# Kernel optimization log

Hardware: AMD Instinct MI355X
Metric: run time of the kernel (lower is better)

The kernel has to match this reference:

```python
import jax, jax.numpy as jnp
import numpy as np

STATE_DIM = 13
HIDDEN = 1024
NUM_SENSORS = 32
BATCH = 131072


def _sensor_locations():
    # Replicates the torch buffer construction (linspace over theta/phi on a sphere of radius 2)
    sensor_range = 2.0
    theta = np.linspace(0.0, 2.0 * np.pi, NUM_SENSORS // 2, dtype=np.float64)
    phi = np.linspace(0.0, np.pi, 2, dtype=np.float64)
    sensors = []
    for p in phi:
        for t in theta:
            sensors.append([sensor_range * np.sin(p) * np.cos(t),
                            sensor_range * np.sin(p) * np.sin(t),
                            sensor_range * np.cos(p)])
    return jnp.asarray(np.asarray(sensors[:NUM_SENSORS], dtype=np.float32))


def setup_inputs() -> dict:
    key = jax.random.key(0)
    ks = jax.random.split(key, 24)

    def lin(kw, fan_in, fan_out):
        # torch nn.Linear default init: U(-1/sqrt(fan_in), 1/sqrt(fan_in))
        bound = 1.0 / np.sqrt(fan_in)
        w = jax.random.uniform(kw, (fan_in, fan_out), jnp.float32, -bound, bound)
        return w

    def bias(kb, fan_in, fan_out):
        bound = 1.0 / np.sqrt(fan_in)
        return jax.random.uniform(kb, (fan_out,), jnp.float32, -bound, bound)

    branch_in = NUM_SENSORS * (STATE_DIM + 4)  # 544
    h2, h4, h8 = HIDDEN // 2, HIDDEN // 4, HIDDEN // 8
    inp = {
        "state": jax.random.normal(ks[0], (BATCH, STATE_DIM), jnp.float32),
        "action": jax.random.normal(ks[1], (BATCH, 4), jnp.float32),
        "sensor_locations": _sensor_locations(),
        "bw1": lin(ks[2], branch_in, HIDDEN), "bb1": bias(ks[3], branch_in, HIDDEN),
        "bw2": lin(ks[4], HIDDEN, h2), "bb2": bias(ks[5], HIDDEN, h2),
        "bw3": lin(ks[6], h2, h4), "bb3": bias(ks[7], h2, h4),
        "tw1": lin(ks[8], 3, h4), "tb1": bias(ks[9], 3, h4),
        "tw2": lin(ks[10], h4, h4), "tb2": bias(ks[11], h4, h4),
        "qw1": lin(ks[12], 3, h8), "qb1": bias(ks[13], 3, h8),
        "qw2": lin(ks[14], h8, STATE_DIM), "qb2": bias(ks[15], h8, STATE_DIM),
        "pw": lin(ks[16], h4, STATE_DIM), "pb": bias(ks[17], h4, STATE_DIM),
        "residual_weight": jnp.float32(0.1),
    }
    return inp


def reference(state, action, sensor_locations,
              bw1, bb1, bw2, bb2, bw3, bb3,
              tw1, tb1, tw2, tb2,
              qw1, qb1, qw2, qb2,
              pw, pb, residual_weight):
    B = state.shape[0]
    pos = state[:, :3]

    # Vectorized sensor encoding (replaces the 32-iteration python loop):
    # distance [B, S, 1], weight = exp(-d/0.5)
    diff = sensor_locations[None, :, :] - pos[:, None, :]          # [B, S, 3]
    dist = jnp.linalg.norm(diff, axis=-1, keepdims=True)           # [B, S, 1]
    w = jnp.exp(-dist / 0.5)                                       # [B, S, 1]
    sv = jnp.concatenate([state[:, None, :] * w,
                          action[:, None, :] * w], axis=-1)        # [B, S, sd+4]
    enc = sv.reshape(B, -1)                                        # [B, S*(sd+4)]

    # Branch net (dropout is identity in eval mode)
    h = jax.nn.relu(enc @ bw1 + bb1)
    h = jax.nn.relu(h @ bw2 + bb2)
    branch = h @ bw3 + bb3                                         # [B, hidden//4]

    # Trunk net on eval coords
    t = jnp.tanh(pos @ tw1 + tb1)
    trunk = jnp.tanh(t @ tw2 + tb2)                                # [B, hidden//4]

    interaction = branch * trunk
    output_delta = interaction @ pw + pb                           # [B, state_dim]

    b = jax.nn.relu(pos @ qw1 + qb1)
    bias_out = b @ qw2 + qb2                                       # [B, state_dim]

    next_state = state + residual_weight * (output_delta + bias_out)

    # Quaternion normalization for dims 3:7 (state_dim >= 7)
    quat = next_state[:, 3:7]
    qn = jnp.linalg.norm(quat, axis=1, keepdims=True)
    next_state = next_state.at[:, 3:7].set(quat / (qn + 1e-8))
    return next_state
```

## Files before the change

kernel.cpp:

```cpp
#include <hip/hip_runtime.h>
#include <hip/hip_bf16.h>
#include <hip/hip_fp8.h>

#define B_TOTAL 131072

typedef __attribute__((ext_vector_type(8))) short short8;
typedef __attribute__((ext_vector_type(4))) float f32x4;
typedef __attribute__((ext_vector_type(16))) unsigned char uchar16;
typedef __attribute__((ext_vector_type(4))) int int4v;
typedef __attribute__((ext_vector_type(8))) int int8v;
typedef unsigned int uint;

#define MFMA(a,b,c) __builtin_amdgcn_mfma_f32_16x16x32_bf16(a,b,c,0,0,0)
#define MFMA8(a,b,c) __builtin_amdgcn_mfma_f32_16x16x32_fp8_fp8(a,b,c,0,0,0)
#define MFMAS(a,b,c) __builtin_amdgcn_mfma_scale_f32_16x16x128_f8f6f4( \
    a, b, c, 0, 0, 0, 0x7F7F7F7F, 0, 0x7F7F7F7F)

union V8U { int8v v; int4v h[2]; };

__device__ __forceinline__ short f2bf(float f) {
  union { float f; uint u; } x; x.f = f;
  uint r = x.u + 0x7fffu + ((x.u >> 16) & 1u);
  return (short)(r >> 16);
}
__device__ __forceinline__ unsigned char f2fp8(float v) {
  union { __hip_fp8_e4m3 q; unsigned char b; } u;
  u.q = __hip_fp8_e4m3(v);
  return u.b;
}
__device__ __forceinline__ float ftanh(float x) {
  float e = __builtin_amdgcn_exp2f(x * 2.8853900817779268f);
  return 1.f - 2.f * __builtin_amdgcn_rcpf(e + 1.f);
}

__device__ __forceinline__ void gl_lds16(const void* g, void* l) {
  __builtin_amdgcn_global_load_lds((const __attribute__((address_space(1))) uint*)g,
                                   (__attribute__((address_space(3))) uint*)l, 16, 0, 0);
}
__device__ __forceinline__ int swz8(int c, int r) { return (c & ~7) | ((c ^ r) & 7); }

__global__ __launch_bounds__(256)
void prep(const float* __restrict__ bw1, const float* __restrict__ bw2,
          const float* __restrict__ bw3, const float* __restrict__ tw2,
          const float* __restrict__ pw, const float* __restrict__ qw2,
          unsigned char* __restrict__ w1f, unsigned char* __restrict__ w2f,
          unsigned char* __restrict__ w3r, short* __restrict__ w4r,
          short* __restrict__ pwT, short* __restrict__ qw2T) {
  __shared__ float tile[32][33];
  int b = blockIdx.x;
  if (b == 1344) {
    for (int t = threadIdx.x; t < 6144; t += 256) {
      if (t < 4096) { int c = t >> 8, k = t & 255;
        pwT[t] = (c < 13) ? f2bf(pw[k * 13 + c]) : (short)0; }
      else { int i = t - 4096; int c = i >> 7, j = i & 127;
        qw2T[i] = (c < 13) ? f2bf(qw2[j * 13 + c]) : (short)0; }
    }
    return;
  }
  const float* src; int K, N, mat;
  if (b < 640)       { src = bw1; K = 544;  N = 1024; mat = 0; }
  else if (b < 1152) { b -= 640;  src = bw2; K = 1024; N = 512;  mat = 1; }
  else if (b < 1280) { b -= 1152; src = bw3; K = 512;  N = 256;  mat = 2; }
  else               { b -= 1280; src = tw2; K = 256;  N = 256;  mat = 3; }
  const int ntk = (mat == 0) ? 20 : (mat == 1) ? 32 : (mat == 2) ? 16 : 8;
  const int tn = b / ntk, tk = b % ntk;
  const int k0 = tk * 32, n0 = tn * 32;
  const int tx = threadIdx.x & 31, ty = threadIdx.x >> 5;
#pragma unroll
  for (int rr = 0; rr < 32; rr += 8) {
    int k = k0 + ty + rr;
    tile[ty + rr][tx] = (k < K) ? src[(long)k * N + n0 + tx] : 0.f;
  }
  __syncthreads();
#pragma unroll
  for (int rr = 0; rr < 32; rr += 8) {
    int nl = ty + rr;
    int n = n0 + nl, k = k0 + tx;
    float v = tile[tx][nl];
    if (mat == 0) w1f[(long)n * 640 + k] = f2fp8(v);
    else if (mat == 1) w2f[(long)n * 1024 + k] = f2fp8(v);
    else {
      int ks = k >> 5, fq = (k >> 3) & 3, j = k & 7;
      int wb = n >> 5, hf = (n >> 4) & 1, fr = n & 15;
      long idx = (long)(((ks * 8 + wb) * 2 + hf) * 4 + fq) * 128 + fr * 8 + j;
      if (mat == 2) w3r[idx] = f2fp8(v);
      else          w4r[idx] = f2bf(v);
    }
  }
}

__global__ __launch_bounds__(256)
void enc_k(const float* __restrict__ state, const float* __restrict__ action,
           const float* __restrict__ sensors, unsigned char* __restrict__ enc) {
  __shared__ float sval[64][17];
  __shared__ float wexp[64][32];
  __shared__ float sens[96];
  const int tid = threadIdx.x;
  const int rb = blockIdx.x * 64;
  if (tid < 96) sens[tid] = sensors[tid];
  for (int i = tid; i < 64 * 17; i += 256) {
    const int r = i / 17, c = i % 17;
    const long grow = rb + r;
    sval[r][c] = (c < 13) ? state[grow * 13 + c] : action[grow * 4 + (c - 13)];
  }
  __syncthreads();
  for (int i = tid; i < 64 * 32; i += 256) {
    const int r = i >> 5, s = i & 31;
    const float dx = sens[s*3+0] - sval[r][0];
    const float dy = sens[s*3+1] - sval[r][1];
    const float dz = sens[s*3+2] - sval[r][2];
    wexp[r][s] = __expf(-2.0f * sqrtf(dx*dx + dy*dy + dz*dz));
  }
  __syncthreads();
  for (int i = tid; i < 64 * 40; i += 256) {
    const int r = i / 40, c16 = i % 40;
    uchar16 v;
#pragma unroll
    for (int j = 0; j < 16; ++j) {
      const int k = c16 * 16 + j;
      unsigned char o = 0;
      if (k < 544) { const int s = k / 17, c = k % 17; o = f2fp8(sval[r][c] * wexp[r][s]); }
      v[j] = o;
    }
    *(uchar16*)&enc[((long)(rb + r)) * 640 + c16 * 16] = v;
  }
}

template<int N, int K, int ACT>
__global__ __launch_bounds__(256, 2)
void gemm_mx(const unsigned char* __restrict__ A, const unsigned char* __restrict__ Bt,
             const float* __restrict__ bias, unsigned char* __restrict__ C) {
  constexpr int NT = K / 128;
  constexpr int NTN = N / 128;
  __shared__ __align__(16) unsigned char As[2][128 * 128];
  __shared__ __align__(16) unsigned char Bs[2][128 * 128];
  const int tid = threadIdx.x;
  const int wave = tid >> 6;
  const int lane = tid & 63;
  const int Mtiles = gridDim.x / NTN;
  const int bid = blockIdx.x;
  const int xcd = bid & 7, seq = bid >> 3;
  const int tm = xcd * (Mtiles >> 3) + seq / NTN;
  const int tn = seq % NTN;
  const long arow0 = (long)tm * 128;
  const long brow0 = (long)tn * 128;

  auto stage = [&](int b, int kt) {
    const int k0 = kt * 128;
#pragma unroll
    for (int it = 0; it < 4; ++it) {
      const int ch = it * 256 + tid;
      const int row = ch >> 3;
      const int cs = (ch & 7) ^ (row & 7);
      gl_lds16(A + (arow0 + row) * (long)K + k0 + cs * 16, &As[b][ch * 16]);
      gl_lds16(Bt + (brow0 + row) * (long)K + k0 + cs * 16, &Bs[b][ch * 16]);
    }
  };

  const int wr = (wave >> 1) * 64;
  const int wc = (wave & 1) * 64;
  const int fr = lane & 15;
  const int fg = lane >> 4;

  f32x4 acc[4][4] = {};

  stage(0, 0);
  for (int kt = 0; kt < NT; ++kt) {
    const int cur = kt & 1;
    __syncthreads();
    if (kt + 1 < NT) stage(cur ^ 1, kt + 1);
    const unsigned char* Ab = As[cur];
    const unsigned char* Bb = Bs[cur];
    int8v av[4], bv2[4];
#pragma unroll
    for (int m = 0; m < 4; ++m) {
      const int row = wr + m * 16 + fr;
      const int p0 = (2 * fg) ^ (row & 7);
      V8U u;
      u.h[0] = *(const int4v*)&Ab[row * 128 + (p0 << 4)];
      u.h[1] = *(const int4v*)&Ab[row * 128 + ((p0 ^ 1) << 4)];
      av[m] = u.v;
    }
#pragma unroll
    for (int n = 0; n < 4; ++n) {
      const int col = wc + n * 16 + fr;
      const int p0 = (2 * fg) ^ (col & 7);
      V8U u;
      u.h[0] = *(const int4v*)&Bb[col * 128 + (p0 << 4)];
      u.h[1] = *(const int4v*)&Bb[col * 128 + ((p0 ^ 1) << 4)];
      bv2[n] = u.v;
    }
#pragma unroll
    for (int m = 0; m < 4; ++m)
#pragma unroll
      for (int n = 0; n < 4; ++n)
        acc[m][n] = MFMAS(av[m], bv2[n], acc[m][n]);
  }

  float bv[4];
#pragma unroll
  for (int n = 0; n < 4; ++n) bv[n] = bias[tn * 128 + wc + n * 16 + fr];
#pragma unroll
  for (int m = 0; m < 4; ++m)
#pragma unroll
    for (int n = 0; n < 4; ++n) {
      const long col = brow0 + wc + n * 16 + fr;
#pragma unroll
      for (int r = 0; r < 4; ++r) {
        const long row = arow0 + wr + m * 16 + fg * 4 + r;
        float v = acc[m][n][r] + bv[n];
        if (ACT == 1) v = fmaxf(v, 0.f);
        C[row * (long)N + col] = f2fp8(v);
      }
    }
}

__global__ __launch_bounds__(512, 4)
void k2(const unsigned char* __restrict__ h2, const float* __restrict__ state,
        const float* __restrict__ tw1, const float* __restrict__ tb1,
        const unsigned char* __restrict__ w3r, const float* __restrict__ bb3,
        const short* __restrict__ w4r, const float* __restrict__ tb2,
        const short* __restrict__ pwT, const float* __restrict__ qw1,
        const short* __restrict__ qw2T, const float* __restrict__ qb1,
        const float* __restrict__ pb, const float* __restrict__ qb2,
        const float* __restrict__ rwp, float* __restrict__ out) {
  __shared__ __align__(16) char lds[77824];
  char*  h2S = lds;
  short* tS  = (short*)(lds + 32768);
  short* pwS = (short*)(lds + 65536);
  short* q2S = (short*)(lds + 73728);
  float* prS = (float*)(lds + 16384);
  float* pr2S= (float*)(lds + 20480);

  const int tid = threadIdx.x, wave = tid >> 6, lane = tid & 63;
  const int fr = lane & 15, fg = lane >> 4;
  const long rb = (long)blockIdx.x * 64;

#pragma unroll
  for (int it = 0; it < 4; ++it) {
    int ch = it * 512 + tid;
    int row = ch >> 5, c = ch & 31;
    gl_lds16(h2 + (rb + row) * 512 + ((c ^ (row & 7)) << 4), h2S + ch * 16);
  }
  { int row = tid >> 5, c = tid & 31;
    gl_lds16(pwT + (long)row * 256 + swz8(c, row) * 8, (char*)pwS + tid * 16); }
  if (tid < 256) { int row = tid >> 4, c = tid & 15;
    gl_lds16(qw2T + (long)row * 128 + swz8(c, row) * 8, (char*)q2S + tid * 16); }

  long long bb[4][2];
#pragma unroll
  for (int ks = 0; ks < 4; ++ks) {
    bb[ks][0] = *(const long long*)&w3r[(long)((ks * 8 + wave) * 2 + 0) * 512 + lane * 8];
    bb[ks][1] = *(const long long*)&w3r[(long)((ks * 8 + wave) * 2 + 1) * 512 + lane * 8];
  }

  for (int i = tid; i < 64 * 32; i += 512) {
    int r = i >> 5, c8 = i & 31;
    float p0 = state[(rb + r) * 13 + 0], p1 = state[(rb + r) * 13 + 1], p2 = state[(rb + r) * 13 + 2];
    short8 v;
#pragma unroll
    for (int j = 0; j < 8; ++j) {
      int jj = c8 * 8 + j;
      v[j] = f2bf(ftanh(p0 * tw1[jj] + p1 * tw1[256 + jj] + p2 * tw1[512 + jj] + tb1[jj]));
    }
    *(short8*)&tS[(r * 32 + swz8(c8, r)) * 8] = v;
  }
  __syncthreads();

  f32x4 acc3[4][2] = {};
#pragma unroll
  for (int ks = 0; ks < 16; ++ks) {
    long long a[4];
#pragma unroll
    for (int mf = 0; mf < 4; ++mf) {
      int row = mf * 16 + fr;
      int c16 = (ks * 2 + (fg >> 1)) ^ (row & 7);
      a[mf] = *(const long long*)&h2S[row * 512 + (c16 << 4) + ((fg & 1) << 3)];
    }
    const long long c0 = bb[ks & 3][0], c1 = bb[ks & 3][1];
    if (ks + 4 < 16) {
      bb[ks & 3][0] = *(const long long*)&w3r[(long)(((ks + 4) * 8 + wave) * 2 + 0) * 512 + lane * 8];
      bb[ks & 3][1] = *(const long long*)&w3r[(long)(((ks + 4) * 8 + wave) * 2 + 1) * 512 + lane * 8];
    }
#pragma unroll
    for (int mf = 0; mf < 4; ++mf) {
      acc3[mf][0] = MFMA8(a[mf], c0, acc3[mf][0]);
      acc3[mf][1] = MFMA8(a[mf], c1, acc3[mf][1]);
    }
  }

  short8 bb4[2][2];
#pragma unroll
  for (int ks = 0; ks < 2; ++ks) {
    bb4[ks][0] = *(const short8*)&w4r[(long)((ks * 8 + wave) * 2 + 0) * 512 + lane * 8];
    bb4[ks][1] = *(const short8*)&w4r[(long)((ks * 8 + wave) * 2 + 1) * 512 + lane * 8];
  }
  f32x4 accT[4][2] = {};
#pragma unroll
  for (int ks = 0; ks < 8; ++ks) {
    const short8 c0 = bb4[ks & 1][0], c1 = bb4[ks & 1][1];
    if (ks + 2 < 8) {
      bb4[ks & 1][0] = *(const short8*)&w4r[(long)(((ks + 2) * 8 + wave) * 2 + 0) * 512 + lane * 8];
      bb4[ks & 1][1] = *(const short8*)&w4r[(long)(((ks + 2) * 8 + wave) * 2 + 1) * 512 + lane * 8];
    }
#pragma unroll
    for (int mf = 0; mf < 4; ++mf) {
      int row = mf * 16 + fr;
      short8 aF = *(const short8*)&tS[row * 256 + swz8(ks * 4 + fg, row) * 8];
      accT[mf][0] = MFMA(aF, c0, accT[mf][0]);
      accT[mf][1] = MFMA(aF, c1, accT[mf][1]);
    }
  }
  __syncthreads();

#pragma unroll
  for (int nf = 0; nf < 2; ++nf) {
    int col = wave * 32 + nf * 16 + fr;
    float b3 = bb3[col], t2 = tb2[col];
#pragma unroll
    for (int mf = 0; mf < 4; ++mf)
#pragma unroll
      for (int i = 0; i < 4; ++i) {
        int row = mf * 16 + fg * 4 + i;
        float br = acc3[mf][nf][i] + b3;
        float tr = ftanh(accT[mf][nf][i] + t2);
        tS[row * 256 + swz8(col >> 3, row) * 8 + (col & 7)] = f2bf(br * tr);
      }
  }
  __syncthreads();

  if (wave < 4) {
    int row = wave * 16 + fr;
    f32x4 accP = {0.f, 0.f, 0.f, 0.f};
#pragma unroll
    for (int ks = 0; ks < 8; ++ks) {
      short8 a = *(const short8*)&tS[row * 256 + swz8(ks * 4 + fg, row) * 8];
      short8 b = *(const short8*)&pwS[fr * 256 + swz8(ks * 4 + fg, fr) * 8];
      accP = MFMA(a, b, accP);
    }
#pragma unroll
    for (int i = 0; i < 4; ++i)
      prS[(wave * 16 + fg * 4 + i) * 16 + fr] = accP[i];
  } else {
    int row = (wave - 4) * 16 + fr;
    float p0 = state[(rb + row) * 13 + 0], p1 = state[(rb + row) * 13 + 1],
          p2 = state[(rb + row) * 13 + 2];
    f32x4 accQ = {0.f, 0.f, 0.f, 0.f};
#pragma unroll
    for (int ks = 0; ks < 4; ++ks) {
      short8 a;
#pragma unroll
      for (int j = 0; j < 8; ++j) {
        int jj = (ks * 4 + fg) * 8 + j;
        float hv = fmaxf(p0 * qw1[jj] + p1 * qw1[128 + jj] + p2 * qw1[256 + jj] + qb1[jj], 0.f);
        a[j] = f2bf(hv);
      }
      short8 b = *(const short8*)&q2S[fr * 128 + swz8(ks * 4 + fg, fr) * 8];
      accQ = MFMA(a, b, accQ);
    }
#pragma unroll
    for (int i = 0; i < 4; ++i)
      pr2S[((wave - 4) * 16 + fg * 4 + i) * 16 + fr] = accQ[i];
  }
  __syncthreads();

  if (tid < 64) {
    int r = tid;
    float rw = rwp[0];
    float ns[13];
#pragma unroll
    for (int c = 0; c < 13; ++c)
      ns[c] = state[(rb + r) * 13 + c] + rw * (prS[r * 16 + c] + pr2S[r * 16 + c] + pb[c] + qb2[c]);
    float qn = sqrtf(ns[3] * ns[3] + ns[4] * ns[4] + ns[5] * ns[5] + ns[6] * ns[6]) + 1e-8f;
#pragma unroll
    for (int c = 3; c < 7; ++c) ns[c] /= qn;
#pragma unroll
    for (int c = 0; c < 13; ++c) out[(rb + r) * 13 + c] = ns[c];
  }
}

extern "C" void kernel_launch(void* const* d_in, const int* in_sizes, int n_in,
                              void* d_out, int out_size, void* d_ws, size_t ws_size,
                              hipStream_t stream) {
  const float* state  = (const float*)d_in[0];
  const float* action = (const float*)d_in[1];
  const float* sensors= (const float*)d_in[2];
  const float* bw1 = (const float*)d_in[3];
  const float* bb1 = (const float*)d_in[4];
  const float* bw2 = (const float*)d_in[5];
  const float* bb2 = (const float*)d_in[6];
  const float* bw3 = (const float*)d_in[7];
  const float* bb3 = (const float*)d_in[8];
  const float* tw1 = (const float*)d_in[9];
  const float* tb1 = (const float*)d_in[10];
  const float* tw2 = (const float*)d_in[11];
  const float* tb2 = (const float*)d_in[12];
  const float* qw1 = (const float*)d_in[13];
  const float* qb1 = (const float*)d_in[14];
  const float* qw2 = (const float*)d_in[15];
  const float* qb2 = (const float*)d_in[16];
  const float* pw  = (const float*)d_in[17];
  const float* pb  = (const float*)d_in[18];
  const float* rw  = (const float*)d_in[19];
  float* out = (float*)d_out;

  char* p = (char*)d_ws;
  unsigned char* w1f = (unsigned char*)p; p += (size_t)1024 * 640;
  unsigned char* w2f = (unsigned char*)p; p += (size_t)512 * 1024;
  unsigned char* w3r = (unsigned char*)p; p += (size_t)256 * 512;
  short* w4r = (short*)p;          p += (size_t)256 * 256 * 2;
  short* pwT = (short*)p;          p += (size_t)16 * 256 * 2;
  short* qw2T= (short*)p;          p += (size_t)16 * 128 * 2;
  const size_t fixed = (size_t)(p - (char*)d_ws);
  const size_t avail = (ws_size > fixed) ? ws_size - fixed : 0;
  long Mc = (long)(avail / 1664) & ~1023L;
  if (Mc > B_TOTAL) Mc = B_TOTAL;
  if (Mc < 1024) return;
  unsigned char* encb = (unsigned char*)p;
  unsigned char* h2b  = (unsigned char*)p;
  unsigned char* h1f  = (unsigned char*)(p + (size_t)Mc * 640);

  prep<<<dim3(1345), dim3(256), 0, stream>>>(bw1, bw2, bw3, tw2, pw, qw2,
                                             w1f, w2f, w3r, w4r, pwT, qw2T);

  for (long r0 = 0; r0 < B_TOTAL; r0 += Mc) {
    long Mr = B_TOTAL - r0; if (Mr > Mc) Mr = Mc;
    enc_k<<<dim3(Mr / 64), dim3(256), 0, stream>>>(state + r0 * 13, action + r0 * 4,
                                                   sensors, encb);
    gemm_mx<1024, 640, 1><<<dim3((Mr / 128) * 8), dim3(256), 0, stream>>>(
        encb, w1f, bb1, h1f);
    gemm_mx<512, 1024, 1><<<dim3((Mr / 128) * 4), dim3(256), 0, stream>>>(
        h1f, w2f, bb2, h2b);
    k2<<<dim3(Mr / 64), dim3(512), 0, stream>>>(h2b, state + r0 * 13, tw1, tb1,
                                                w3r, bb3, w4r, tb2, pwT, qw1, qw2T,
                                                qb1, pb, qb2, rw, out + r0 * 13);
  }
}
```

Before: 319.7 us.

## Single-buffer GEMM LDS for higher occupancy and use hardware fp8 pack conversion

The MX fp8 GEMM drops its double-buffered LDS staging in favour of a single buffer per operand and raises launch bounds to 4 blocks per CU. Latency is meant to be hidden by running more resident blocks rather than by prefetching within a block. Separately, the software fp8 conversion is replaced with the hardware packed cvt_pk_fp8_f32 builtin, applied two values at a time in both the encoder and the GEMM epilogue. The trade-off is that loads and MFMA no longer overlap within a block, and the higher occupancy target may constrain registers.

```diff
diff --git a/kernel.cpp b/kernel.cpp
--- a/kernel.cpp
+++ b/kernel.cpp
@@ -23,10 +23,24 @@
   uint r = x.u + 0x7fffu + ((x.u >> 16) & 1u);
   return (short)(r >> 16);
 }
-__device__ __forceinline__ unsigned char f2fp8(float v) {
+__device__ __forceinline__ unsigned char f2fp8_sw(float v) {
   union { __hip_fp8_e4m3 q; unsigned char b; } u;
   u.q = __hip_fp8_e4m3(v);
   return u.b;
+}
+__device__ __forceinline__ unsigned char f2fp8(float v) {
+#if __has_builtin(__builtin_amdgcn_cvt_pk_fp8_f32)
+  return (unsigned char)(__builtin_amdgcn_cvt_pk_fp8_f32(v, 0.f, 0, false) & 0xFF);
+#else
+  return f2fp8_sw(v);
+#endif
+}
+__device__ __forceinline__ uint f2fp8x2(float a, float b) {
+#if __has_builtin(__builtin_amdgcn_cvt_pk_fp8_f32)
+  return (uint)__builtin_amdgcn_cvt_pk_fp8_f32(a, b, 0, false) & 0xFFFFu;
+#else
+  return (uint)f2fp8_sw(a) | ((uint)f2fp8_sw(b) << 8);
+#endif
 }
 __device__ __forceinline__ float ftanh(float x) {
   float e = __builtin_amdgcn_exp2f(x * 2.8853900817779268f);
@@ -116,24 +130,27 @@
     const int r = i / 40, c16 = i % 40;
     uchar16 v;
 #pragma unroll
-    for (int j = 0; j < 16; ++j) {
+    for (int j = 0; j < 16; j += 2) {
       const int k = c16 * 16 + j;
-      unsigned char o = 0;
-      if (k < 544) { const int s = k / 17, c = k % 17; o = f2fp8(sval[r][c] * wexp[r][s]); }
-      v[j] = o;
+      float f0 = 0.f, f1 = 0.f;
+      if (k < 544)     { const int s = k / 17, c = k % 17; f0 = sval[r][c] * wexp[r][s]; }
+      if (k + 1 < 544) { const int s = (k + 1) / 17, c = (k + 1) % 17; f1 = sval[r][c] * wexp[r][s]; }
+      uint p = f2fp8x2(f0, f1);
+      v[j] = (unsigned char)(p & 0xFF);
+      v[j + 1] = (unsigned char)(p >> 8);
     }
     *(uchar16*)&enc[((long)(rb + r)) * 640 + c16 * 16] = v;
   }
 }
 
 template<int N, int K, int ACT>
-__global__ __launch_bounds__(256, 2)
+__global__ __launch_bounds__(256, 4)
 void gemm_mx(const unsigned char* __restrict__ A, const unsigned char* __restrict__ Bt,
              const float* __restrict__ bias, unsigned char* __restrict__ C) {
   constexpr int NT = K / 128;
   constexpr int NTN = N / 128;
-  __shared__ __align__(16) unsigned char As[2][128 * 128];
-  __shared__ __align__(16) unsigned char Bs[2][128 * 128];
+  __shared__ __align__(16) unsigned char As[128 * 128];
+  __shared__ __align__(16) unsigned char Bs[128 * 128];
   const int tid = threadIdx.x;
   const int wave = tid >> 6;
   const int lane = tid & 63;
@@ -145,40 +162,33 @@
   const long arow0 = (long)tm * 128;
   const long brow0 = (long)tn * 128;
 
-  auto stage = [&](int b, int kt) {
+  const int wr = (wave >> 1) * 64;
+  const int wc = (wave & 1) * 64;
+  const int fr = lane & 15;
+  const int fg = lane >> 4;
+
+  f32x4 acc[4][4] = {};
+
+  for (int kt = 0; kt < NT; ++kt) {
+    if (kt) __syncthreads();
     const int k0 = kt * 128;
 #pragma unroll
     for (int it = 0; it < 4; ++it) {
       const int ch = it * 256 + tid;
       const int row = ch >> 3;
       const int cs = (ch & 7) ^ (row & 7);
-      gl_lds16(A + (arow0 + row) * (long)K + k0 + cs * 16, &As[b][ch * 16]);
-      gl_lds16(Bt + (brow0 + row) * (long)K + k0 + cs * 16, &Bs[b][ch * 16]);
-    }
-  };
-
-  const int wr = (wave >> 1) * 64;
-  const int wc = (wave & 1) * 64;
-  const int fr = lane & 15;
-  const int fg = lane >> 4;
-
-  f32x4 acc[4][4] = {};
-
-  stage(0, 0);
-  for (int kt = 0; kt < NT; ++kt) {
-    const int cur = kt & 1;
+      gl_lds16(A + (arow0 + row) * (long)K + k0 + cs * 16, &As[ch * 16]);
+      gl_lds16(Bt + (brow0 + row) * (long)K + k0 + cs * 16, &Bs[ch * 16]);
+    }
     __syncthreads();
-    if (kt + 1 < NT) stage(cur ^ 1, kt + 1);
-    const unsigned char* Ab = As[cur];
-    const unsigned char* Bb = Bs[cur];
     int8v av[4], bv2[4];
 #pragma unroll
     for (int m = 0; m < 4; ++m) {
       const int row = wr + m * 16 + fr;
       const int p0 = (2 * fg) ^ (row & 7);
       V8U u;
-      u.h[0] = *(const int4v*)&Ab[row * 128 + (p0 << 4)];
-      u.h[1] = *(const int4v*)&Ab[row * 128 + ((p0 ^ 1) << 4)];
+      u.h[0] = *(const int4v*)&As[row * 128 + (p0 << 4)];
+      u.h[1] = *(const int4v*)&As[row * 128 + ((p0 ^ 1) << 4)];
       av[m] = u.v;
     }
 #pragma unroll
@@ -186,8 +196,8 @@
       const int col = wc + n * 16 + fr;
       const int p0 = (2 * fg) ^ (col & 7);
       V8U u;
-      u.h[0] = *(const int4v*)&Bb[col * 128 + (p0 << 4)];
-      u.h[1] = *(const int4v*)&Bb[col * 128 + ((p0 ^ 1) << 4)];
+      u.h[0] = *(const int4v*)&Bs[col * 128 + (p0 << 4)];
+      u.h[1] = *(const int4v*)&Bs[col * 128 + ((p0 ^ 1) << 4)];
       bv2[n] = u.v;
     }
 #pragma unroll
@@ -203,14 +213,16 @@
 #pragma unroll
   for (int m = 0; m < 4; ++m)
 #pragma unroll
-    for (int n = 0; n < 4; ++n) {
-      const long col = brow0 + wc + n * 16 + fr;
-#pragma unroll
-      for (int r = 0; r < 4; ++r) {
-        const long row = arow0 + wr + m * 16 + fg * 4 + r;
-        float v = acc[m][n][r] + bv[n];
-        if (ACT == 1) v = fmaxf(v, 0.f);
-        C[row * (long)N + col] = f2fp8(v);
+    for (int r = 0; r < 4; ++r) {
+      const long row = arow0 + wr + m * 16 + fg * 4 + r;
+#pragma unroll
+      for (int np = 0; np < 2; ++np) {
+        float v0 = acc[m][2 * np][r] + bv[2 * np];
+        float v1 = acc[m][2 * np + 1][r] + bv[2 * np + 1];
+        if (ACT == 1) { v0 = fmaxf(v0, 0.f); v1 = fmaxf(v1, 0.f); }
+        uint p = f2fp8x2(v0, v1);
+        C[row * (long)N + brow0 + wc + (2 * np) * 16 + fr] = (unsigned char)(p & 0xFF);
+        C[row * (long)N + brow0 + wc + (2 * np + 1) * 16 + fr] = (unsigned char)(p >> 8);
       }
     }
 }
```

Result: slower. 579.9 us (+81.4%).

## Pre-swizzle GEMM weights into MFMA fragment order and load B directly into registers

Applied to the files above, without the earlier changes.

The prep kernel now writes bw1/bw2 in fp8 as per-16-column, per-128-K records laid out in MFMA operand order, so each lane can read its 32-byte B fragment with two contiguous 16-byte global loads. The GEMM drops the B shared-memory tile and its LDS staging and reads, and double-buffers B fragments in registers alongside the async A staging. This halves LDS use per block and removes LDS traffic for B. In exchange it adds register pressure and makes B reads depend on global/L2 latency without LDS sharing between the two waves that use the same columns.

```diff
diff --git a/kernel.cpp b/kernel.cpp
--- a/kernel.cpp
+++ b/kernel.cpp
@@ -43,7 +43,7 @@
 void prep(const float* __restrict__ bw1, const float* __restrict__ bw2,
           const float* __restrict__ bw3, const float* __restrict__ tw2,
           const float* __restrict__ pw, const float* __restrict__ qw2,
-          unsigned char* __restrict__ w1f, unsigned char* __restrict__ w2f,
+          unsigned char* __restrict__ w1r, unsigned char* __restrict__ w2r,
           unsigned char* __restrict__ w3r, short* __restrict__ w4r,
           short* __restrict__ pwT, short* __restrict__ qw2T) {
   __shared__ float tile[32][33];
@@ -77,9 +77,13 @@
     int nl = ty + rr;
     int n = n0 + nl, k = k0 + tx;
     float v = tile[tx][nl];
-    if (mat == 0) w1f[(long)n * 640 + k] = f2fp8(v);
-    else if (mat == 1) w2f[(long)n * 1024 + k] = f2fp8(v);
-    else {
+    if (mat == 0 || mat == 1) {
+      const int NTk = (mat == 0) ? 5 : 8;
+      unsigned char* dst = (mat == 0) ? w1r : w2r;
+      const long rec = (long)(n >> 4) * NTk + (k >> 7);
+      const int ln = ((k >> 5) & 3) * 16 + (n & 15);
+      dst[rec * 2048 + ln * 32 + (k & 31)] = f2fp8(v);
+    } else {
       int ks = k >> 5, fq = (k >> 3) & 3, j = k & 7;
       int wb = n >> 5, hf = (n >> 4) & 1, fr = n & 15;
       long idx = (long)(((ks * 8 + wb) * 2 + hf) * 4 + fq) * 128 + fr * 8 + j;
@@ -128,12 +132,11 @@
 
 template<int N, int K, int ACT>
 __global__ __launch_bounds__(256, 2)
-void gemm_mx(const unsigned char* __restrict__ A, const unsigned char* __restrict__ Bt,
+void gemm_mx(const unsigned char* __restrict__ A, const unsigned char* __restrict__ Br,
              const float* __restrict__ bias, unsigned char* __restrict__ C) {
   constexpr int NT = K / 128;
   constexpr int NTN = N / 128;
   __shared__ __align__(16) unsigned char As[2][128 * 128];
-  __shared__ __align__(16) unsigned char Bs[2][128 * 128];
   const int tid = threadIdx.x;
   const int wave = tid >> 6;
   const int lane = tid & 63;
@@ -145,7 +148,12 @@
   const long arow0 = (long)tm * 128;
   const long brow0 = (long)tn * 128;
 
-  auto stage = [&](int b, int kt) {
+  const int wr = (wave >> 1) * 64;
+  const int wc = (wave & 1) * 64;
+  const int fr = lane & 15;
+  const int fg = lane >> 4;
+
+  auto stageA = [&](int b, int kt) {
     const int k0 = kt * 128;
 #pragma unroll
     for (int it = 0; it < 4; ++it) {
@@ -153,25 +161,33 @@
       const int row = ch >> 3;
       const int cs = (ch & 7) ^ (row & 7);
       gl_lds16(A + (arow0 + row) * (long)K + k0 + cs * 16, &As[b][ch * 16]);
-      gl_lds16(Bt + (brow0 + row) * (long)K + k0 + cs * 16, &Bs[b][ch * 16]);
     }
   };
 
-  const int wr = (wave >> 1) * 64;
-  const int wc = (wave & 1) * 64;
-  const int fr = lane & 15;
-  const int fg = lane >> 4;
+  const unsigned char* bbase = Br + ((long)(tn * 8 + (wc >> 4)) * NT) * 2048 + lane * 32;
+  int8v bvb[2][4];
+  auto bload = [&](int buf, int kt) {
+#pragma unroll
+    for (int n = 0; n < 4; ++n) {
+      const unsigned char* p = bbase + ((long)n * NT + kt) * 2048;
+      V8U u;
+      u.h[0] = *(const int4v*)p;
+      u.h[1] = *(const int4v*)(p + 16);
+      bvb[buf][n] = u.v;
+    }
+  };
 
   f32x4 acc[4][4] = {};
 
-  stage(0, 0);
+  stageA(0, 0);
+  bload(0, 0);
+#pragma unroll
   for (int kt = 0; kt < NT; ++kt) {
     const int cur = kt & 1;
     __syncthreads();
-    if (kt + 1 < NT) stage(cur ^ 1, kt + 1);
+    if (kt + 1 < NT) { stageA(cur ^ 1, kt + 1); bload(cur ^ 1, kt + 1); }
     const unsigned char* Ab = As[cur];
-    const unsigned char* Bb = Bs[cur];
-    int8v av[4], bv2[4];
+    int8v av[4];
 #pragma unroll
     for (int m = 0; m < 4; ++m) {
       const int row = wr + m * 16 + fr;
@@ -182,19 +198,10 @@
       av[m] = u.v;
     }
 #pragma unroll
-    for (int n = 0; n < 4; ++n) {
-      const int col = wc + n * 16 + fr;
-      const int p0 = (2 * fg) ^ (col & 7);
-      V8U u;
-      u.h[0] = *(const int4v*)&Bb[col * 128 + (p0 << 4)];
-      u.h[1] = *(const int4v*)&Bb[col * 128 + ((p0 ^ 1) << 4)];
-      bv2[n] = u.v;
-    }
-#pragma unroll
     for (int m = 0; m < 4; ++m)
 #pragma unroll
       for (int n = 0; n < 4; ++n)
-        acc[m][n] = MFMAS(av[m], bv2[n], acc[m][n]);
+        acc[m][n] = MFMAS(av[m], bvb[cur][n], acc[m][n]);
   }
 
   float bv[4];
@@ -405,8 +412,8 @@
   float* out = (float*)d_out;
 
   char* p = (char*)d_ws;
-  unsigned char* w1f = (unsigned char*)p; p += (size_t)1024 * 640;
-  unsigned char* w2f = (unsigned char*)p; p += (size_t)512 * 1024;
+  unsigned char* w1r = (unsigned char*)p; p += (size_t)1024 * 640;
+  unsigned char* w2r = (unsigned char*)p; p += (size_t)512 * 1024;
   unsigned char* w3r = (unsigned char*)p; p += (size_t)256 * 512;
   short* w4r = (short*)p;          p += (size_t)256 * 256 * 2;
   short* pwT = (short*)p;          p += (size_t)16 * 256 * 2;
@@ -421,16 +428,16 @@
   unsigned char* h1f  = (unsigned char*)(p + (size_t)Mc * 640);
 
   prep<<<dim3(1345), dim3(256), 0, stream>>>(bw1, bw2, bw3, tw2, pw, qw2,
-                                             w1f, w2f, w3r, w4r, pwT, qw2T);
+                                             w1r, w2r, w3r, w4r, pwT, qw2T);
 
   for (long r0 = 0; r0 < B_TOTAL; r0 += Mc) {
     long Mr = B_TOTAL - r0; if (Mr > Mc) Mr = Mc;
     enc_k<<<dim3(Mr / 64), dim3(256), 0, stream>>>(state + r0 * 13, action + r0 * 4,
                                                    sensors, encb);
     gemm_mx<1024, 640, 1><<<dim3((Mr / 128) * 8), dim3(256), 0, stream>>>(
-        encb, w1f, bb1, h1f);
+        encb, w1r, bb1, h1f);
     gemm_mx<512, 1024, 1><<<dim3((Mr / 128) * 4), dim3(256), 0, stream>>>(
-        h1f, w2f, bb2, h2b);
+        h1f, w2r, bb2, h2b);
     k2<<<dim3(Mr / 64), dim3(512), 0, stream>>>(h2b, state + r0 * 13, tw1, tb1,
                                                 w3r, bb3, w4r, tb2, pwT, qw1, qw2T,
                                                 qb1, pb, qb2, rw, out + r0 * 13);
```

After: 304.9 us (median of 3 runs). 1.05x faster.
